# Performance work log

Hardware: AMD Instinct MI355X
Metric: run time of the kernel (lower is better)

Reference implementation:

```python
import jax, jax.numpy as jnp
import numpy as np

N_HEADS = 16

def setup_inputs() -> dict:
    key = jax.random.key(0)
    ks = jax.random.split(key, 5)
    C = 1024
    B, T = 2, 2048
    s_in = 1.0 / np.sqrt(C)
    x = jax.random.normal(ks[0], (B, T, C), dtype=jnp.float32)
    W_qkv = jax.random.normal(ks[1], (C, 3 * C), dtype=jnp.float32) * s_in
    b_qkv = jnp.zeros((3 * C,), dtype=jnp.float32)
    W_proj = jax.random.normal(ks[2], (C, C), dtype=jnp.float32) * s_in
    b_proj = jnp.zeros((C,), dtype=jnp.float32)
    return {"x": x, "W_qkv": W_qkv, "b_qkv": b_qkv, "W_proj": W_proj, "b_proj": b_proj}

def reference(x, W_qkv, b_qkv, W_proj, b_proj):
    B, T, C = x.shape
    H = N_HEADS
    D = C // H  # head dim
    qkv = x @ W_qkv + b_qkv                      # [B,T,3C]
    q, k, v = jnp.split(qkv, 3, axis=-1)
    # [B,T,C] -> [B,H,T,D]
    q = q.reshape(B, T, H, D).transpose(0, 2, 1, 3)
    k = k.reshape(B, T, H, D).transpose(0, 2, 1, 3)
    v = v.reshape(B, T, H, D).transpose(0, 2, 1, 3)
    scale = 1.0 / np.sqrt(D)
    att = jnp.einsum('bhqd,bhkd->bhqk', q, k) * scale  # [B,H,T,T]
    causal = jnp.tril(jnp.ones((T, T), dtype=bool))
    att = jnp.where(causal[None, None], att, -jnp.inf)
    att = jax.nn.softmax(att, axis=-1)
    y = jnp.einsum('bhqk,bhkd->bhqd', att, v)    # [B,H,T,D]
    y = y.transpose(0, 2, 1, 3).reshape(B, T, C)
    return y @ W_proj + b_proj
```

## Files before the change

kernel.cpp:

```cpp
#include <hip/hip_runtime.h>
#include <hip/hip_bf16.h>
#include <stdint.h>

#define DEVI __device__ __forceinline__

typedef __attribute__((ext_vector_type(8))) short bf16x8;
typedef __attribute__((ext_vector_type(4))) float f32x4;
typedef __attribute__((ext_vector_type(4))) short short4v;
typedef __attribute__((ext_vector_type(4))) float float4v;
typedef __attribute__((ext_vector_type(2))) unsigned int uint2v;

#define QSCALE 0.1803368801111204f

DEVI unsigned short f2bf(float f) {
  union { float f; unsigned u; } v; v.f = f;
  unsigned r = v.u + 0x7FFFu + ((v.u >> 16) & 1u);
  return (unsigned short)(r >> 16);
}

DEVI float bf2f(unsigned short u) {
  union { unsigned u; float f; } v; v.u = ((unsigned)u) << 16; return v.f;
}

DEVI unsigned cvt_pk_bf16(float lo, float hi) {
  unsigned r;
  asm("v_cvt_pk_bf16_f32 %0, %1, %2" : "=v"(r) : "v"(lo), "v"(hi));
  return r;
}

DEVI void async16(unsigned short* lds, const unsigned short* g) {
  __builtin_amdgcn_global_load_lds(
      (const __attribute__((address_space(1))) void*)g,
      (__attribute__((address_space(3))) void*)lds, 16, 0, 0);
}

DEVI int xcd_swz_flat() {
  int orig = (int)blockIdx.x + (int)gridDim.x * (int)blockIdx.y;
  int cpx = ((int)gridDim.x * (int)gridDim.y) >> 3;
  return (orig & 7) * cpx + (orig >> 3);
}

__device__ const signed char JOB_X[24] =
    {15,15, 7,14,14,13,13, 6,12,12,11,11, 5,10,10, 9, 9, 4, 8, 8, 3, 2, 1, 0};
__device__ const signed char JOB_S[24] =
    { 0, 1, 2, 0, 1, 0, 1, 2, 0, 1, 0, 1, 2, 0, 1, 0, 1, 2, 0, 1, 2, 2, 2, 2};

__global__ void k_f32_to_bf16(const float* __restrict__ in,
                              unsigned short* __restrict__ out, int n4) {
  int i = blockIdx.x * 256 + threadIdx.x;
  if (i < n4) {
    float4v f = *reinterpret_cast<const float4v*>(in + (size_t)i * 4);
    short4v o;
#pragma unroll
    for (int j = 0; j < 4; ++j) o[j] = (short)f2bf(f[j]);
    *reinterpret_cast<short4v*>(out + (size_t)i * 4) = o;
  }
}

__global__ void k_wt2(const float* __restrict__ Wq, const float* __restrict__ Wp,
                      unsigned short* __restrict__ WqT, unsigned short* __restrict__ WpT) {
  __shared__ float tile[32][33];
  const int bx = (int)blockIdx.x;
  const float* W;
  unsigned short* Wt;
  int N, n0;
  if (bx < 96) { W = Wq; Wt = WqT; N = 3072; n0 = bx * 32; }
  else         { W = Wp; Wt = WpT; N = 1024; n0 = (bx - 96) * 32; }
  const int K = 1024, k0 = (int)blockIdx.y * 32;
  int r = threadIdx.x >> 5, c = threadIdx.x & 31;
#pragma unroll
  for (int i = 0; i < 4; ++i)
    tile[r + i * 8][c] = W[(size_t)(k0 + r + i * 8) * N + n0 + c];
  __syncthreads();
#pragma unroll
  for (int i = 0; i < 4; ++i)
    Wt[(size_t)(n0 + r + i * 8) * K + k0 + c] = f2bf(tile[c][r + i * 8]);
}

DEVI void stage_ab(unsigned short* AsB, unsigned short* BsB,
                   const unsigned short* Ab, const unsigned short* Bb,
                   int K, int k0, int tid) {
  int row = tid >> 2, cc = (tid & 3) * 8;
  async16(&AsB[tid * 8], Ab + (size_t)row * K + k0 + cc);
  async16(&BsB[tid * 8], Bb + (size_t)row * K + k0 + cc);
}

__global__ __launch_bounds__(512)
void k_gemm(const unsigned short* __restrict__ A,
            const unsigned short* __restrict__ Bt,
            const float* __restrict__ bias,
            unsigned short* __restrict__ qkv,
            unsigned short* __restrict__ vt,
            int M, int N, int K) {
  __shared__ __align__(16) unsigned short As[2][128 * 32];
  __shared__ __align__(16) unsigned short Bs[2][128 * 32];
  const int tid = threadIdx.x;
  const int swzf = xcd_swz_flat();
  const int m0 = (swzf / (int)gridDim.x) * 128, n0 = (swzf % (int)gridDim.x) * 128;
  const int lane = tid & 63, w = tid >> 6;
  const int wr = (w >> 2) * 64, wc = (w & 3) * 32;
  const int lr = lane & 15, lg = lane >> 4;
  f32x4 acc[4][2] = {};
  const unsigned short* Ab = A + (size_t)m0 * K;
  const unsigned short* Bb = Bt + (size_t)n0 * K;

  const int ns = K >> 5;
  stage_ab(As[0], Bs[0], Ab, Bb, K, 0, tid);
  stage_ab(As[1], Bs[1], Ab, Bb, K, 32, tid);
  asm volatile("s_waitcnt vmcnt(2)" ::: "memory");
  __builtin_amdgcn_s_barrier();
  __builtin_amdgcn_sched_barrier(0);

  for (int s = 0; s < ns; ++s) {
    const int cur = s & 1;
    bf16x8 af[4], bfr[2];
#pragma unroll
    for (int m = 0; m < 4; ++m)
      af[m] = *reinterpret_cast<const bf16x8*>(&As[cur][(wr + m * 16 + lr) * 32 + lg * 8]);
#pragma unroll
    for (int n = 0; n < 2; ++n)
      bfr[n] = *reinterpret_cast<const bf16x8*>(&Bs[cur][(wc + n * 16 + lr) * 32 + lg * 8]);
#pragma unroll
    for (int m = 0; m < 4; ++m)
#pragma unroll
      for (int n = 0; n < 2; ++n)
        acc[m][n] = __builtin_amdgcn_mfma_f32_16x16x32_bf16(af[m], bfr[n], acc[m][n], 0, 0, 0);
    __builtin_amdgcn_s_barrier();
    const int ks = (s + 2 < ns) ? (s + 2) * 32 : 0;
    stage_ab(As[cur], Bs[cur], Ab, Bb, K, ks, tid);
    asm volatile("s_waitcnt vmcnt(2)" ::: "memory");
    __builtin_amdgcn_s_barrier();
    __builtin_amdgcn_sched_barrier(0);
  }
#pragma unroll
  for (int n = 0; n < 2; ++n) {
    int col = n0 + wc + n * 16 + lr;
    float bv = bias[col];
    int sel = col >> 10, cc = col & 1023;
    int h = cc >> 6, d = cc & 63;
    if (sel < 2) {
      float sc = (sel == 0) ? QSCALE : 1.0f;
#pragma unroll
      for (int m = 0; m < 4; ++m) {
#pragma unroll
        for (int r = 0; r < 4; ++r) {
          int row = m0 + wr + m * 16 + lg * 4 + r;
          int bh = ((row >> 11) << 4) + h;
          int t = row & 2047;
          qkv[((size_t)(sel * 32 + bh) * 2048 + t) * 64 + d] = f2bf((acc[m][n][r] + bv) * sc);
        }
      }
    } else {
#pragma unroll
      for (int m = 0; m < 4; ++m) {
        int row0 = m0 + wr + m * 16 + lg * 4;
        int bh = ((row0 >> 11) << 4) + h;
        int t0 = row0 & 2047;
        short4v pk;
#pragma unroll
        for (int r = 0; r < 4; ++r) pk[r] = (short)f2bf(acc[m][n][r] + bv);
        *reinterpret_cast<short4v*>(&vt[((size_t)(bh * 64 + d)) * 2048 + t0]) = pk;
      }
    }
  }
}

__global__ __launch_bounds__(256)
void k_gemmP(const unsigned short* __restrict__ A,
             const unsigned short* __restrict__ Bt,
             const float* __restrict__ bias,
             float* __restrict__ O, int M, int N, int K) {
  __shared__ __align__(16) unsigned short As[2][128 * 32];
  __shared__ __align__(16) unsigned short Bs[2][64 * 32];
  const int tid = threadIdx.x;
  const int swzf = xcd_swz_flat();
  const int m0 = (swzf / (int)gridDim.x) * 128, n0 = (swzf % (int)gridDim.x) * 64;
  const int lane = tid & 63, w = tid >> 6;
  const int wr = (w >> 1) * 64, wc = (w & 1) * 32;
  const int lr = lane & 15, lg = lane >> 4;
  f32x4 acc[4][2] = {};
  const unsigned short* Ab = A + (size_t)m0 * K;
  const unsigned short* Bb = Bt + (size_t)n0 * K;

  auto stage = [&](unsigned short* AsB, unsigned short* BsB, int k0) {
#pragma unroll
    for (int it = 0; it < 2; ++it) {
      int c = it * 256 + tid;
      int row = c >> 2, cc = (c & 3) * 8;
      async16(&AsB[c * 8], Ab + (size_t)row * K + k0 + cc);
    }
    int row = tid >> 2, cc = (tid & 3) * 8;
    async16(&BsB[tid * 8], Bb + (size_t)row * K + k0 + cc);
  };

  const int ns = K >> 5;
  stage(As[0], Bs[0], 0);
  stage(As[1], Bs[1], 32);
  asm volatile("s_waitcnt vmcnt(3)" ::: "memory");
  __builtin_amdgcn_s_barrier();
  __builtin_amdgcn_sched_barrier(0);

  for (int s = 0; s < ns; ++s) {
    const int cur = s & 1;
    bf16x8 af[4], bfr[2];
#pragma unroll
    for (int m = 0; m < 4; ++m)
      af[m] = *reinterpret_cast<const bf16x8*>(&As[cur][(wr + m * 16 + lr) * 32 + lg * 8]);
#pragma unroll
    for (int n = 0; n < 2; ++n)
      bfr[n] = *reinterpret_cast<const bf16x8*>(&Bs[cur][(wc + n * 16 + lr) * 32 + lg * 8]);
#pragma unroll
    for (int m = 0; m < 4; ++m)
#pragma unroll
      for (int n = 0; n < 2; ++n)
        acc[m][n] = __builtin_amdgcn_mfma_f32_16x16x32_bf16(af[m], bfr[n], acc[m][n], 0, 0, 0);
    __builtin_amdgcn_s_barrier();
    const int ks = (s + 2 < ns) ? (s + 2) * 32 : 0;
    stage(As[cur], Bs[cur], ks);
    asm volatile("s_waitcnt vmcnt(3)" ::: "memory");
    __builtin_amdgcn_s_barrier();
    __builtin_amdgcn_sched_barrier(0);
  }
#pragma unroll
  for (int n = 0; n < 2; ++n) {
    int col = n0 + wc + n * 16 + lr;
    float bv = bias[col];
#pragma unroll
    for (int m = 0; m < 4; ++m)
#pragma unroll
      for (int r = 0; r < 4; ++r) {
        int row = m0 + wr + m * 16 + lg * 4 + r;
        O[(size_t)row * N + col] = acc[m][n][r] + bv;
      }
  }
}

DEVI void stage_kv(unsigned short* KsB, unsigned short* VsB,
                   const unsigned short* Kbh, const unsigned short* Vbh,
                   int k0, int tid, int srow, int gcol) {
  async16(&KsB[tid * 8], Kbh + (size_t)(k0 + srow) * 64 + gcol);
  async16(&VsB[tid * 8], Vbh + (size_t)srow * 2048 + k0 + gcol);
}

__global__ __launch_bounds__(512)
void k_attn(const unsigned short* __restrict__ Qg,
            const unsigned short* __restrict__ Kg,
            const unsigned short* __restrict__ Vtg,
            unsigned short* __restrict__ Y,
            unsigned short* __restrict__ po,
            float2* __restrict__ pml) {
  __shared__ __align__(16) unsigned short Ks[2][64 * 64];
  __shared__ __align__(16) unsigned short Vs[2][64 * 64];
  __shared__ __align__(16) unsigned short Ps[8][16 * 64];
  const int orig = (int)blockIdx.x;
  const int xcd = orig & 7;
  const int p = orig >> 3;
  const int bh = xcd * 4 + (p & 3);
  const int rank = p >> 2;
  const int x = JOB_X[rank];
  const int sf = JOB_S[rank];
  const int nsplit = (sf == 2) ? 1 : 2;
  const int s = (sf == 2) ? 0 : sf;
  const int tA = (nsplit == 2 && s == 1) ? (x + 1) : 0;
  const int tB = (nsplit == 2 && s == 0) ? (x + 1) : (2 * x + 2);
  const int tid = threadIdx.x, lane = tid & 63, w = tid >> 6;
  const int lr = lane & 15, lg = lane >> 4;
  const int swz = (lane & 7) * 8;
  const int psw = (lr & 7) * 8;
  const unsigned short* Kbh = Kg + (size_t)bh * 2048 * 64;
  const unsigned short* Vbh = Vtg + (size_t)bh * 64 * 2048;

  const int qw = x * 128 + w * 16;
  const unsigned short* Qrow = Qg + ((size_t)bh * 2048 + qw + lr) * 64;
  bf16x8 qa0 = *reinterpret_cast<const bf16x8*>(&Qrow[lg * 8]);
  bf16x8 qa1 = *reinterpret_cast<const bf16x8*>(&Qrow[32 + lg * 8]);

  float l_run = 0.f;
  f32x4 o[4] = {};

  const int srow = tid >> 3;
  const int gcol = ((tid & 7) ^ (srow & 7)) * 8;

  stage_kv(Ks[0], Vs[0], Kbh, Vbh, tA * 64, tid, srow, gcol);
  stage_kv(Ks[1], Vs[1], Kbh, Vbh, (tA + 1) * 64, tid, srow, gcol);
  asm volatile("s_waitcnt vmcnt(2)" ::: "memory");
  __builtin_amdgcn_s_barrier();
  __builtin_amdgcn_sched_barrier(0);

  for (int t = tA; t < tB; ++t) {
    const int cur = (t - tA) & 1;
    const int k0 = t * 64;
    if (k0 <= qw + 15) {
      const unsigned short* KsC = Ks[cur];
      const unsigned short* VsC = Vs[cur];

      f32x4 sc[4];
      __builtin_amdgcn_s_setprio(1);
#pragma unroll
      for (int n = 0; n < 4; ++n) {
        bf16x8 kb0 = *reinterpret_cast<const bf16x8*>(&KsC[(n * 16 + lr) * 64 + ((lg * 8) ^ swz)]);
        bf16x8 kb1 = *reinterpret_cast<const bf16x8*>(&KsC[(n * 16 + lr) * 64 + ((32 + lg * 8) ^ swz)]);
        f32x4 z = {0.f, 0.f, 0.f, 0.f};
        z = __builtin_amdgcn_mfma_f32_16x16x32_bf16(kb0, qa0, z, 0, 0, 0);
        z = __builtin_amdgcn_mfma_f32_16x16x32_bf16(kb1, qa1, z, 0, 0, 0);
        sc[n] = z;
      }
      __builtin_amdgcn_s_setprio(0);
      if (k0 + 63 > qw) {
        const int klim = qw + lr - k0 - lg * 4;
#pragma unroll
        for (int n = 0; n < 4; ++n)
#pragma unroll
          for (int r = 0; r < 4; ++r)
            if (n * 16 + r > klim) sc[n][r] = -1e30f;
      }
#pragma unroll
      for (int n = 0; n < 4; ++n)
#pragma unroll
        for (int r = 0; r < 4; ++r) {
          sc[n][r] = __builtin_exp2f(sc[n][r]);
          l_run += sc[n][r];
        }
#pragma unroll
      for (int n = 0; n < 4; ++n) {
        uint2v pk;
        pk[0] = cvt_pk_bf16(sc[n][0], sc[n][1]);
        pk[1] = cvt_pk_bf16(sc[n][2], sc[n][3]);
        *reinterpret_cast<uint2v*>(&Ps[w][lr * 64 + ((n * 16 + lg * 4) ^ psw)]) = pk;
      }
      __builtin_amdgcn_s_setprio(1);
#pragma unroll
      for (int jj = 0; jj < 2; ++jj) {
        bf16x8 pa = *reinterpret_cast<const bf16x8*>(&Ps[w][lr * 64 + ((jj * 32 + lg * 8) ^ psw)]);
#pragma unroll
        for (int n = 0; n < 4; ++n) {
          bf16x8 vb = *reinterpret_cast<const bf16x8*>(
              &VsC[(n * 16 + lr) * 64 + ((jj * 32 + lg * 8) ^ swz)]);
          o[n] = __builtin_amdgcn_mfma_f32_16x16x32_bf16(pa, vb, o[n], 0, 0, 0);
        }
      }
      __builtin_amdgcn_s_setprio(0);
    }
    __builtin_amdgcn_s_barrier();
    {
      const int ts = (t + 2 < tB) ? (t + 2) : tA;
      stage_kv(Ks[cur], Vs[cur], Kbh, Vbh, ts * 64, tid, srow, gcol);
    }
    asm volatile("s_waitcnt vmcnt(2)" ::: "memory");
    __builtin_amdgcn_s_barrier();
    __builtin_amdgcn_sched_barrier(0);
  }
  l_run += __shfl_xor(l_run, 16, 64);
  l_run += __shfl_xor(l_run, 32, 64);
  const int b = bh >> 4, h = bh & 15;
  if (nsplit == 1) {
    float rl = 1.0f / l_run;
    float rlo[4];
#pragma unroll
    for (int r = 0; r < 4; ++r) rlo[r] = __shfl(rl, lg * 4 + r, 64);
#pragma unroll
    for (int r = 0; r < 4; ++r) {
      int t = qw + lg * 4 + r;
#pragma unroll
      for (int n = 0; n < 4; ++n)
        Y[((size_t)(b * 2048 + t)) * 1024 + h * 64 + n * 16 + lr] = f2bf(o[n][r] * rlo[r]);
    }
  } else {
    const int g = bh * 8 + (x - 8);
    if (lg == 0) {
      float2 v; v.x = 0.f; v.y = l_run;
      pml[(g * 2 + s) * 128 + w * 16 + lr] = v;
    }
    float oo[4][4];
#pragma unroll
    for (int r = 0; r < 4; ++r)
#pragma unroll
      for (int n = 0; n < 4; ++n) oo[r][n] = o[n][r];
    if (s == 0) {
#pragma unroll
      for (int r = 0; r < 4; ++r) {
        int t = qw + lg * 4 + r;
#pragma unroll
        for (int n = 0; n < 4; ++n)
          Y[((size_t)(b * 2048 + t)) * 1024 + h * 64 + n * 16 + lr] = f2bf(oo[r][n]);
      }
    } else {
#pragma unroll
      for (int r = 0; r < 4; ++r) {
        int row = w * 16 + lg * 4 + r;
#pragma unroll
        for (int n = 0; n < 4; ++n)
          po[((size_t)g * 128 + row) * 64 + n * 16 + lr] = f2bf(oo[r][n]);
      }
    }
  }
}

__global__ __launch_bounds__(256)
void k_merge(unsigned short* __restrict__ Y,
             const unsigned short* __restrict__ po,
             const float2* __restrict__ pml) {
  const int g = (int)blockIdx.x;
  const int bh = g >> 3, x = (g & 7) + 8;
  const int b = bh >> 4, h = bh & 15;
  const int row = threadIdx.x >> 1;
  const int d0 = ((int)threadIdx.x & 1) * 32;
  float2 p0 = pml[(g * 2 + 0) * 128 + row];
  float2 p1 = pml[(g * 2 + 1) * 128 + row];
  float m = fmaxf(p0.x, p1.x);
  float a0 = __builtin_exp2f(p0.x - m), a1 = __builtin_exp2f(p1.x - m);
  float inv = 1.0f / (p0.y * a0 + p1.y * a1);
  float c0 = a0 * inv, c1 = a1 * inv;
  size_t yb = ((size_t)(b * 2048 + x * 128 + row)) * 1024 + h * 64 + d0;
  size_t pb = ((size_t)g * 128 + row) * 64 + d0;
#pragma unroll
  for (int i = 0; i < 4; ++i) {
    bf16x8 yv = *reinterpret_cast<const bf16x8*>(&Y[yb + i * 8]);
    bf16x8 pv = *reinterpret_cast<const bf16x8*>(&po[pb + i * 8]);
    bf16x8 ov;
#pragma unroll
    for (int jj = 0; jj < 8; ++jj)
      ov[jj] = (short)f2bf(bf2f((unsigned short)yv[jj]) * c0 +
                           bf2f((unsigned short)pv[jj]) * c1);
    *reinterpret_cast<bf16x8*>(&Y[yb + i * 8]) = ov;
  }
}

extern "C" void kernel_launch(void* const* d_in, const int* in_sizes, int n_in,
                              void* d_out, int out_size, void* d_ws, size_t ws_size,
                              hipStream_t stream) {
  const float* x     = (const float*)d_in[0];
  const float* Wqkv  = (const float*)d_in[1];
  const float* bqkv  = (const float*)d_in[2];
  const float* Wproj = (const float*)d_in[3];
  const float* bproj = (const float*)d_in[4];
  float* out = (float*)d_out;

  uint8_t* ws = (uint8_t*)d_ws;
  unsigned short* xb     = (unsigned short*)(ws);
  unsigned short* wqkvT  = (unsigned short*)(ws + ((size_t)8  << 20));
  unsigned short* wprojT = (unsigned short*)(ws + ((size_t)14 << 20));
  unsigned short* qkvb   = (unsigned short*)(ws + ((size_t)16 << 20));
  unsigned short* vt     = (unsigned short*)(ws + ((size_t)32 << 20));
  unsigned short* po     = (unsigned short*)(ws + ((size_t)8  << 20));
  float2*         pml    = (float2*)(ws + ((size_t)12 << 20));

  k_f32_to_bf16<<<4096, 256, 0, stream>>>(x, xb, 1048576);
  k_wt2<<<dim3(128, 32), 256, 0, stream>>>(Wqkv, Wproj, wqkvT, wprojT);
  k_gemm<<<dim3(24, 32), 512, 0, stream>>>(xb, wqkvT, bqkv, qkvb, vt, 4096, 3072, 1024);
  k_attn<<<dim3(768, 1), 512, 0, stream>>>(qkvb, qkvb + (size_t)32 * 2048 * 64, vt, xb, po, pml);
  k_merge<<<dim3(256, 1), 256, 0, stream>>>(xb, po, pml);
  k_gemmP<<<dim3(16, 32), 256, 0, stream>>>(xb, wprojT, bproj, out, 4096, 1024, 1024);
}
```

Before: 108.4 us.

## Fuse prep kernels, shrink projection GEMM tile, rebalance attention job schedule

Merges the x-to-bf16 conversion and the weight transpose into one launch, removing one kernel launch. Halves the output-projection GEMM M tile from 128 to 64, doubling its grid to 1024 blocks so more CUs stay busy. Replaces the attention work table with a per-slot table that places different causal work sizes together on each XCD, aiming for better load balance. The smaller GEMM tile lowers data reuse per block and adds more loads overall.

```diff
diff --git a/kernel.cpp b/kernel.cpp
--- a/kernel.cpp
+++ b/kernel.cpp
@@ -40,33 +40,34 @@
   return (orig & 7) * cpx + (orig >> 3);
 }
 
-__device__ const signed char JOB_X[24] =
-    {15,15, 7,14,14,13,13, 6,12,12,11,11, 5,10,10, 9, 9, 4, 8, 8, 3, 2, 1, 0};
-__device__ const signed char JOB_S[24] =
-    { 0, 1, 2, 0, 1, 0, 1, 2, 0, 1, 0, 1, 2, 0, 1, 0, 1, 2, 0, 1, 2, 2, 2, 2};
-
-__global__ void k_f32_to_bf16(const float* __restrict__ in,
-                              unsigned short* __restrict__ out, int n4) {
-  int i = blockIdx.x * 256 + threadIdx.x;
-  if (i < n4) {
-    float4v f = *reinterpret_cast<const float4v*>(in + (size_t)i * 4);
+__device__ const signed char TTX[8][3] = {
+  {15,15, 0},{ 7,13, 1},{14,12, 2},{14,10, 3},
+  {13,10, 8},{ 6, 9, 9},{12,11, 8},{11, 5, 4}};
+__device__ const signed char TTS[8][3] = {
+  {0,1,2},{2,0,2},{0,0,2},{1,0,2},{1,1,0},{2,0,1},{1,0,1},{1,2,2}};
+
+__global__ void k_prep(const float* __restrict__ x, unsigned short* __restrict__ xb,
+                       const float* __restrict__ Wq, const float* __restrict__ Wp,
+                       unsigned short* __restrict__ WqT, unsigned short* __restrict__ WpT) {
+  __shared__ float tile[32][33];
+  const int id = (int)blockIdx.x;
+  if (id < 4096) {
+    int i = id * 256 + (int)threadIdx.x;
+    float4v f = *reinterpret_cast<const float4v*>(x + (size_t)i * 4);
     short4v o;
 #pragma unroll
     for (int j = 0; j < 4; ++j) o[j] = (short)f2bf(f[j]);
-    *reinterpret_cast<short4v*>(out + (size_t)i * 4) = o;
-  }
-}
-
-__global__ void k_wt2(const float* __restrict__ Wq, const float* __restrict__ Wp,
-                      unsigned short* __restrict__ WqT, unsigned short* __restrict__ WpT) {
-  __shared__ float tile[32][33];
-  const int bx = (int)blockIdx.x;
+    *reinterpret_cast<short4v*>(xb + (size_t)i * 4) = o;
+    return;
+  }
+  const int flat = id - 4096;
+  const int bx = flat & 127, k0 = (flat >> 7) * 32;
   const float* W;
   unsigned short* Wt;
   int N, n0;
   if (bx < 96) { W = Wq; Wt = WqT; N = 3072; n0 = bx * 32; }
   else         { W = Wp; Wt = WpT; N = 1024; n0 = (bx - 96) * 32; }
-  const int K = 1024, k0 = (int)blockIdx.y * 32;
+  const int K = 1024;
   int r = threadIdx.x >> 5, c = threadIdx.x & 31;
 #pragma unroll
   for (int i = 0; i < 4; ++i)
@@ -170,54 +171,49 @@
              const unsigned short* __restrict__ Bt,
              const float* __restrict__ bias,
              float* __restrict__ O, int M, int N, int K) {
-  __shared__ __align__(16) unsigned short As[2][128 * 32];
+  __shared__ __align__(16) unsigned short As[2][64 * 32];
   __shared__ __align__(16) unsigned short Bs[2][64 * 32];
   const int tid = threadIdx.x;
   const int swzf = xcd_swz_flat();
-  const int m0 = (swzf / (int)gridDim.x) * 128, n0 = (swzf % (int)gridDim.x) * 64;
+  const int m0 = (swzf / (int)gridDim.x) * 64, n0 = (swzf % (int)gridDim.x) * 64;
   const int lane = tid & 63, w = tid >> 6;
-  const int wr = (w >> 1) * 64, wc = (w & 1) * 32;
+  const int wr = (w >> 1) * 32, wc = (w & 1) * 32;
   const int lr = lane & 15, lg = lane >> 4;
-  f32x4 acc[4][2] = {};
+  f32x4 acc[2][2] = {};
   const unsigned short* Ab = A + (size_t)m0 * K;
   const unsigned short* Bb = Bt + (size_t)n0 * K;
 
   auto stage = [&](unsigned short* AsB, unsigned short* BsB, int k0) {
-#pragma unroll
-    for (int it = 0; it < 2; ++it) {
-      int c = it * 256 + tid;
-      int row = c >> 2, cc = (c & 3) * 8;
-      async16(&AsB[c * 8], Ab + (size_t)row * K + k0 + cc);
-    }
     int row = tid >> 2, cc = (tid & 3) * 8;
+    async16(&AsB[tid * 8], Ab + (size_t)row * K + k0 + cc);
     async16(&BsB[tid * 8], Bb + (size_t)row * K + k0 + cc);
   };
 
   const int ns = K >> 5;
   stage(As[0], Bs[0], 0);
   stage(As[1], Bs[1], 32);
-  asm volatile("s_waitcnt vmcnt(3)" ::: "memory");
+  asm volatile("s_waitcnt vmcnt(2)" ::: "memory");
   __builtin_amdgcn_s_barrier();
   __builtin_amdgcn_sched_barrier(0);
 
   for (int s = 0; s < ns; ++s) {
     const int cur = s & 1;
-    bf16x8 af[4], bfr[2];
-#pragma unroll
-    for (int m = 0; m < 4; ++m)
+    bf16x8 af[2], bfr[2];
+#pragma unroll
+    for (int m = 0; m < 2; ++m)
       af[m] = *reinterpret_cast<const bf16x8*>(&As[cur][(wr + m * 16 + lr) * 32 + lg * 8]);
 #pragma unroll
     for (int n = 0; n < 2; ++n)
       bfr[n] = *reinterpret_cast<const bf16x8*>(&Bs[cur][(wc + n * 16 + lr) * 32 + lg * 8]);
 #pragma unroll
-    for (int m = 0; m < 4; ++m)
+    for (int m = 0; m < 2; ++m)
 #pragma unroll
       for (int n = 0; n < 2; ++n)
         acc[m][n] = __builtin_amdgcn_mfma_f32_16x16x32_bf16(af[m], bfr[n], acc[m][n], 0, 0, 0);
     __builtin_amdgcn_s_barrier();
     const int ks = (s + 2 < ns) ? (s + 2) * 32 : 0;
     stage(As[cur], Bs[cur], ks);
-    asm volatile("s_waitcnt vmcnt(3)" ::: "memory");
+    asm volatile("s_waitcnt vmcnt(2)" ::: "memory");
     __builtin_amdgcn_s_barrier();
     __builtin_amdgcn_sched_barrier(0);
   }
@@ -226,7 +222,7 @@
     int col = n0 + wc + n * 16 + lr;
     float bv = bias[col];
 #pragma unroll
-    for (int m = 0; m < 4; ++m)
+    for (int m = 0; m < 2; ++m)
 #pragma unroll
       for (int r = 0; r < 4; ++r) {
         int row = m0 + wr + m * 16 + lg * 4 + r;
@@ -255,10 +251,12 @@
   const int orig = (int)blockIdx.x;
   const int xcd = orig & 7;
   const int p = orig >> 3;
-  const int bh = xcd * 4 + (p & 3);
-  const int rank = p >> 2;
-  const int x = JOB_X[rank];
-  const int sf = JOB_S[rank];
+  const int slot = p >> 5;
+  const int q = p & 31;
+  const int type = q >> 2, cpy = q & 3;
+  const int bh = xcd * 4 + ((cpy + slot) & 3);
+  const int x = TTX[type][slot];
+  const int sf = TTS[type][slot];
   const int nsplit = (sf == 2) ? 1 : 2;
   const int s = (sf == 2) ? 0 : sf;
   const int tA = (nsplit == 2 && s == 1) ? (x + 1) : 0;
@@ -445,10 +443,9 @@
   unsigned short* po     = (unsigned short*)(ws + ((size_t)8  << 20));
   float2*         pml    = (float2*)(ws + ((size_t)12 << 20));
 
-  k_f32_to_bf16<<<4096, 256, 0, stream>>>(x, xb, 1048576);
-  k_wt2<<<dim3(128, 32), 256, 0, stream>>>(Wqkv, Wproj, wqkvT, wprojT);
+  k_prep<<<dim3(8192, 1), 256, 0, stream>>>(x, xb, Wqkv, Wproj, wqkvT, wprojT);
   k_gemm<<<dim3(24, 32), 512, 0, stream>>>(xb, wqkvT, bqkv, qkvb, vt, 4096, 3072, 1024);
   k_attn<<<dim3(768, 1), 512, 0, stream>>>(qkvb, qkvb + (size_t)32 * 2048 * 64, vt, xb, po, pml);
   k_merge<<<dim3(256, 1), 256, 0, stream>>>(xb, po, pml);
-  k_gemmP<<<dim3(16, 32), 256, 0, stream>>>(xb, wprojT, bproj, out, 4096, 1024, 1024);
-}
+  k_gemmP<<<dim3(16, 64), 256, 0, stream>>>(xb, wprojT, bproj, out, 4096, 1024, 1024);
+}
```

Result: faster. 103.9 us (-4.2%).
